# Kernel optimization log

Measured on AMD Instinct MI355X. Metric: run time of the kernel, lower is better.

Reference implementation:

```python
import jax, jax.numpy as jnp
import numpy as np


def setup_inputs() -> dict:
    key = jax.random.key(0)
    k1, k2 = jax.random.split(key)
    b, n, d = 8, 8192, 512
    x = jax.random.normal(k1, (b, n, d), dtype=jnp.float32)
    # t holds 2n-2 Toeplitz coefficients per channel; forward only uses the first n rows.
    t = jax.random.normal(k2, (2 * n - 2, d), dtype=jnp.float32)
    return {"x": x, "t": t}


def reference(x, t):
    """Per-channel causal cumulative weighted sum (the math of the naive quadruple loop):
        o[i, u, j] = sum_{v=0}^{u} t[v, j] * x[i, v, j]
    x: (b, n, d), t: (2n-2, d) -> o: (b, n, d)
    """
    n = x.shape[1]
    # broadcast t over batch, fuse elementwise product, then inclusive cumsum along seq
    return jnp.cumsum(x * t[None, :n, :], axis=1)
```

## Files before the change

### kernel.cpp

```cpp
#include <hip/hip_runtime.h>


typedef float f4 __attribute__((ext_vector_type(4)));

#define D  512
#define DV (D / 4)
#define C  128
#define RS 4

__global__ __launch_bounds__(DV * RS) void k_chunksum(
    const float* __restrict__ x, const float* __restrict__ t,
    float* __restrict__ S, int b, int n, int L) {
  const int c  = blockIdx.x / b;
  const int i  = blockIdx.x % b;
  const int jv = threadIdx.x & (DV - 1);
  const int h  = threadIdx.x >> 7;
  const int rows = L / RS;
  const size_t row0 = (size_t)c * L + (size_t)h * rows;
  const f4* xp = (const f4*)x + ((size_t)i * n + row0) * DV + jv;
  const f4* tp = (const f4*)t + row0 * DV + jv;
  f4 acc = {0.f, 0.f, 0.f, 0.f};
#pragma unroll 8
  for (int v = 0; v < rows; ++v) {
    acc += xp[(size_t)v * DV] * tp[(size_t)v * DV];
  }
  __shared__ f4 red[RS][DV];
  red[h][jv] = acc;
  __syncthreads();
  if (h == 0) {
    f4 s = red[0][jv] + red[1][jv] + red[2][jv] + red[3][jv];
    ((f4*)S)[((size_t)c * b + i) * DV + jv] = s;
  }
}

__global__ __launch_bounds__(DV) void k_out(
    const float* __restrict__ x, const float* __restrict__ t,
    const float* __restrict__ S, float* __restrict__ o, int b, int n, int L) {
  const int c  = blockIdx.x / b;
  const int i  = blockIdx.x % b;
  const int jv = threadIdx.x;

  f4 acc = {0.f, 0.f, 0.f, 0.f};
  const f4* Sp = (const f4*)S + (size_t)i * DV + jv;
  const size_t cstride = (size_t)b * DV;
#pragma unroll 8
  for (int cp = 0; cp < c; ++cp) {
    acc += Sp[(size_t)cp * cstride];
  }

  const size_t row0  = (size_t)c * L;
  const size_t xbase = ((size_t)i * n + row0) * DV + jv;
  const f4* xp = (const f4*)x + xbase;
  const f4* tp = (const f4*)t + row0 * DV + jv;
  f4*       op = (f4*)o + xbase;
#pragma unroll 4
  for (int v = 0; v < L; ++v) {
    acc += xp[(size_t)v * DV] * tp[(size_t)v * DV];
    op[(size_t)v * DV] = acc;
  }
}

__global__ __launch_bounds__(256) void k_naive(
    const float* __restrict__ x, const float* __restrict__ t,
    float* __restrict__ o, int b, int n) {
  const int tid = blockIdx.x * 256 + threadIdx.x;
  if (tid >= b * DV) return;
  const int i  = tid / DV;
  const int jv = tid % DV;
  const f4* xp = (const f4*)x + (size_t)i * n * DV + jv;
  const f4* tp = (const f4*)t + jv;
  f4*       op = (f4*)o + (size_t)i * n * DV + jv;
  f4 acc = {0.f, 0.f, 0.f, 0.f};
  for (int v = 0; v < n; ++v) {
    acc += xp[(size_t)v * DV] * tp[(size_t)v * DV];
    op[(size_t)v * DV] = acc;
  }
}

extern "C" void kernel_launch(void* const* d_in, const int* in_sizes, int n_in,
                              void* d_out, int out_size, void* d_ws, size_t ws_size,
                              hipStream_t stream) {
  const float* x = (const float*)d_in[0];
  const float* t = (const float*)d_in[1];
  float*       o = (float*)d_out;

  const long long t_elems = in_sizes[1];
  const int n = (int)((t_elems / D + 2) / 2);
  const int b = (int)((long long)in_sizes[0] / ((long long)n * D));

  const size_t need = (size_t)C * b * D * sizeof(float);

  if (n % C == 0 && (n / C) % RS == 0 && ws_size >= need) {
    const int L = n / C;
    float* S = (float*)d_ws;
    hipLaunchKernelGGL(k_chunksum, dim3(C * b), dim3(DV * RS), 0, stream,
                       x, t, S, b, n, L);
    hipLaunchKernelGGL(k_out, dim3(C * b), dim3(DV), 0, stream,
                       x, t, S, o, b, n, L);
  } else {
    const int threads = b * DV;
    hipLaunchKernelGGL(k_naive, dim3((threads + 255) / 256), dim3(256), 0, stream,
                       x, t, o, b, n);
  }
}
```

Baseline: 303.7 us.

## Fuse chunk-sum and output passes into single-pass scan with decoupled lookback

Replaces the two-kernel chunked scan with one kernel. It takes chunk order from an atomic ticket, publishes per-chunk partial sums with release flags, and spins until all earlier chunks have published. Each thread keeps its 16 products in registers, so x and t are read once instead of twice, and one launch is removed. The cost is a memset of the flags and ticket plus spin-wait serialization between chunks. Each block still re-reads all prior chunk sums linearly.

```diff
diff --git a/kernel.cpp b/kernel.cpp
--- a/kernel.cpp
+++ b/kernel.cpp
@@ -7,6 +7,80 @@
 #define DV (D / 4)
 #define C  128
 #define RS 4
+#define RT 16
+#define NT (DV * RS)
+
+__global__ __launch_bounds__(NT) void k_scan1(
+    const float* __restrict__ x, const float* __restrict__ t,
+    float* S, unsigned int* flags, unsigned int* ticket,
+    float* __restrict__ o, int b, int n) {
+  __shared__ unsigned int s_vid;
+  __shared__ f4 redA[RS][DV];
+  __shared__ f4 redB[RS][DV];
+
+  const int tid = threadIdx.x;
+  if (tid == 0)
+    s_vid = __hip_atomic_fetch_add(ticket, 1u, __ATOMIC_RELAXED,
+                                   __HIP_MEMORY_SCOPE_AGENT);
+  __syncthreads();
+  const int vid = (int)s_vid;
+  const int c   = vid / b;
+  const int i   = vid - c * b;
+  const int jv  = tid & (DV - 1);
+  const int h   = tid >> 7;
+  const int L   = RS * RT;
+
+  const size_t row0 = (size_t)c * L + (size_t)h * RT;
+  const f4* xp = (const f4*)x + ((size_t)i * n + row0) * DV + jv;
+  const f4* tp = (const f4*)t + row0 * DV + jv;
+
+  f4 p[RT];
+  f4 psum = {0.f, 0.f, 0.f, 0.f};
+#pragma unroll
+  for (int r = 0; r < RT; ++r) {
+    p[r] = xp[(size_t)r * DV] * tp[(size_t)r * DV];
+    psum += p[r];
+  }
+  redA[h][jv] = psum;
+  __syncthreads();
+
+  if (h == 0) {
+    f4 s = redA[0][jv] + redA[1][jv] + redA[2][jv] + redA[3][jv];
+    ((f4*)S)[((size_t)c * b + i) * DV + jv] = s;
+  }
+  __syncthreads();
+  if (tid == 0)
+    __hip_atomic_store(&flags[(size_t)c * b + i], 1u, __ATOMIC_RELEASE,
+                       __HIP_MEMORY_SCOPE_AGENT);
+
+  for (int cp = tid; cp < c; cp += NT) {
+    while (__hip_atomic_load(&flags[(size_t)cp * b + i], __ATOMIC_RELAXED,
+                             __HIP_MEMORY_SCOPE_AGENT) == 0u)
+      __builtin_amdgcn_s_sleep(2);
+  }
+  __syncthreads();
+  __threadfence();
+
+  f4 ex = {0.f, 0.f, 0.f, 0.f};
+  const f4* Sp = (const f4*)S + (size_t)i * DV + jv;
+  const size_t cs = (size_t)b * DV;
+#pragma unroll 4
+  for (int cp = h; cp < c; cp += RS)
+    ex += Sp[(size_t)cp * cs];
+  redB[h][jv] = ex;
+  __syncthreads();
+  f4 base = redB[0][jv] + redB[1][jv] + redB[2][jv] + redB[3][jv];
+  for (int hp = 0; hp < h; ++hp)
+    base += redA[hp][jv];
+
+  f4* op = (f4*)o + ((size_t)i * n + row0) * DV + jv;
+  f4 acc = base;
+#pragma unroll
+  for (int r = 0; r < RT; ++r) {
+    acc += p[r];
+    op[(size_t)r * DV] = acc;
+  }
+}
 
 __global__ __launch_bounds__(DV * RS) void k_chunksum(
     const float* __restrict__ x, const float* __restrict__ t,
@@ -39,7 +113,6 @@
   const int c  = blockIdx.x / b;
   const int i  = blockIdx.x % b;
   const int jv = threadIdx.x;
-
   f4 acc = {0.f, 0.f, 0.f, 0.f};
   const f4* Sp = (const f4*)S + (size_t)i * DV + jv;
   const size_t cstride = (size_t)b * DV;
@@ -47,7 +120,6 @@
   for (int cp = 0; cp < c; ++cp) {
     acc += Sp[(size_t)cp * cstride];
   }
-
   const size_t row0  = (size_t)c * L;
   const size_t xbase = ((size_t)i * n + row0) * DV + jv;
   const f4* xp = (const f4*)x + xbase;
@@ -88,9 +160,18 @@
   const int n = (int)((t_elems / D + 2) / 2);
   const int b = (int)((long long)in_sizes[0] / ((long long)n * D));
 
-  const size_t need = (size_t)C * b * D * sizeof(float);
+  const size_t sBytes = (size_t)C * b * D * sizeof(float);
+  const size_t fBytes = (size_t)C * b * sizeof(unsigned);
+  const size_t need1  = sBytes + fBytes + 256;
 
-  if (n % C == 0 && (n / C) % RS == 0 && ws_size >= need) {
+  if (n == C * RS * RT && b >= 1 && ws_size >= need1) {
+    float*        S      = (float*)d_ws;
+    unsigned int* flags  = (unsigned int*)((char*)d_ws + sBytes);
+    unsigned int* ticket = (unsigned int*)((char*)d_ws + sBytes + fBytes);
+    hipMemsetAsync((char*)d_ws + sBytes, 0, fBytes + 64, stream);
+    hipLaunchKernelGGL(k_scan1, dim3(C * b), dim3(NT), 0, stream,
+                       x, t, S, flags, ticket, o, b, n);
+  } else if (n % C == 0 && (n / C) % RS == 0 && ws_size >= sBytes) {
     const int L = n / C;
     float* S = (float*)d_ws;
     hipLaunchKernelGGL(k_chunksum, dim3(C * b), dim3(DV * RS), 0, stream,
```

New measurement: 440.9 us. 45.2% more time.
